# Kernel tuning notes

Hardware: AMD Instinct MI355X
Metric: run time of the kernel (lower is better)

The kernel has to match this reference:

```python
import jax, jax.numpy as jnp
import numpy as np

H, W = 352, 1216
K = 8                 # points_per_pixel (z-buffer depth)
RADIUS_PX = 1.5       # splat radius in pixels
RAD_POW = 2.0         # opts.rad_pow
TAU = 1.0             # opts.tau


def _rasterize(pts):
    # pts: [B,P,3] with xy in NDC [-1,1], z>0.
    # Returns idx [B,H,W,K] int32 (packed point index, -1 = empty),
    # dist2 [B,H,W,K] squared NDC distance to pixel center, and NDC radius r.
    B, P, _ = pts.shape
    r = RADIUS_PX / max(H, W) * 2.0
    hx = int(np.ceil(r * W / 2.0))   # splat half-extent in pixels (x)
    hy = int(np.ceil(r * H / 2.0))   # splat half-extent in pixels (y)
    dy, dx = np.meshgrid(np.arange(-hy, hy + 1), np.arange(-hx, hx + 1), indexing='ij')
    dy = jnp.asarray(dy.ravel()); dx = jnp.asarray(dx.ravel())     # [Wn]
    x, y, z = pts[..., 0], pts[..., 1], pts[..., 2]                # [B,P]
    i0 = jnp.floor((y + 1.0) * 0.5 * H).astype(jnp.int32)
    j0 = jnp.floor((x + 1.0) * 0.5 * W).astype(jnp.int32)
    ii = i0[..., None] + dy                                        # [B,P,Wn]
    jj = j0[..., None] + dx
    xc = (jj + 0.5) * (2.0 / W) - 1.0                              # pixel centers (NDC)
    yc = (ii + 0.5) * (2.0 / H) - 1.0
    d2 = (x[..., None] - xc) ** 2 + (y[..., None] - yc) ** 2
    valid = (ii >= 0) & (ii < H) & (jj >= 0) & (jj < W) & (d2 < r * r) & (z[..., None] > 0)
    NPIX = B * H * W
    pix = jnp.where(valid, (jnp.arange(B)[:, None, None] * H + ii) * W + jj, NPIX)
    pid = jnp.broadcast_to((jnp.arange(B)[:, None] * P + jnp.arange(P)[None, :])[..., None], pix.shape)
    pixf = pix.reshape(-1)
    zf = jnp.broadcast_to(z[..., None], pix.shape).reshape(-1)
    d2f = d2.reshape(-1)
    pidf = pid.reshape(-1)
    # sort candidates by (pixel, z): gives nearest-first z-buffer ordering per pixel
    order = jnp.lexsort((zf, pixf))
    pixs, d2s, pids = pixf[order], d2f[order], pidf[order]
    first = jnp.searchsorted(pixs, pixs, side='left')
    rank = jnp.arange(pixs.shape[0]) - first      # z-rank within each pixel
    keep = (rank < K) & (pixs < NPIX)
    tp = jnp.where(keep, pixs, NPIX)              # sentinel row NPIX collects rejects
    tr = jnp.where(keep, rank, 0)
    idx = jnp.full((NPIX + 1, K), -1, jnp.int32).at[tp, tr].set(
        jnp.where(keep, pids, -1).astype(jnp.int32))
    dist2 = jnp.zeros((NPIX + 1, K), pts.dtype).at[tp, tr].set(
        jnp.where(keep, d2s, jnp.zeros((), pts.dtype)))
    return idx[:NPIX].reshape(B, H, W, K), dist2[:NPIX].reshape(B, H, W, K), r


def _forward(pts3D, src):
    B, C, P = src.shape
    idx, dist2, r = _rasterize(pts3D)
    dist = dist2 / (r ** RAD_POW)
    alphas = (1.0 - jnp.sqrt(jnp.clip(dist, 0.001, 1.0))) ** TAU   # [B,H,W,K]
    feats = src.transpose(0, 2, 1).reshape(B * P, C)               # features_packed [B*P,C]
    acc = jnp.zeros((B, H, W, C), src.dtype)
    for k in range(K):   # fixed small depth-layer loop: weighted_sum compositing
        ik = idx[..., k]
        wk = jnp.where(ik >= 0, alphas[..., k], 0.0)
        acc = acc + wk[..., None] * feats[jnp.clip(ik, 0)]
    return acc.transpose(0, 3, 1, 2)                               # [B,C,H,W]


def setup_inputs():
    key = jax.random.key(0)
    k1, k2, k3 = jax.random.split(key, 3)
    B, P, C = 2, 65536, 64
    xy = jax.random.uniform(k1, (B, P, 2), minval=-1.0, maxval=1.0)
    z = jax.random.uniform(k2, (B, P, 1), minval=0.5, maxval=20.0)
    pts3D = jnp.concatenate([xy, z], axis=-1)
    src = jax.random.normal(k3, (B, C, P), dtype=jnp.float32)
    return {"pts3D": pts3D, "src": src}


def reference(pts3D, src):
    return _forward(pts3D, src)
```

## Files before the change

### kernel.cpp

```cpp
#include <hip/hip_runtime.h>
#include <cstdint>
#include <cstddef>

#define HH 352
#define WW 1216
#define KK 8
#define PP 65536
#define BB 2
#define CC 64

#define RD (1.5 / 1216.0 * 2.0)


__global__ __launch_bounds__(256) void scatter_kernel(const float* __restrict__ pts,
                                                      unsigned int* __restrict__ slots) {
    const int tid = blockIdx.x * blockDim.x + threadIdx.x;
    const int b = tid >> 16;
    const float x = pts[tid * 3 + 0];
    const float y = pts[tid * 3 + 1];
    const float z = pts[tid * 3 + 2];
    if (!(z > 0.f)) return;

    const int i0 = (int)floorf((y + 1.f) * 0.5f * (float)HH);
    if (i0 < 0 || i0 >= HH) return;
    const int j0 = (int)floorf((x + 1.f) * 0.5f * (float)WW);

    const float yc = ((float)i0 + 0.5f) * (2.f / (float)HH) - 1.f;
    const float dyv = y - yc;
    const float dy2 = dyv * dyv;
    const float r2 = (float)(RD * RD);

    unsigned int fb = __float_as_uint(z) >> 13;
    fb = fb < 0x1F800u ? 0x1F800u : fb;
    fb = fb > 0x217FFu ? 0x217FFu : fb;
    const unsigned int key = ((fb - 0x1F800u) << 17) | (unsigned int)tid;

    const unsigned int rowbase = (unsigned int)(b * HH + i0) * WW;

    #pragma unroll
    for (int dx = -1; dx <= 1; ++dx) {
        const int jj = j0 + dx;
        if (jj < 0 || jj >= WW) continue;
        const float xc = ((float)jj + 0.5f) * (2.f / (float)WW) - 1.f;
        const float dxv = x - xc;
        if (!(dxv * dxv + dy2 < r2)) continue;

        unsigned int* s = slots + (size_t)(rowbase + jj) * KK;
        unsigned int cur = key;
        #pragma unroll
        for (int k = 0; k < KK; ++k) {
            unsigned int old = atomicMin(&s[k], cur);
            if (old & 0x80000000u) break;
            cur = old > cur ? old : cur;
        }
    }
}

__global__ __launch_bounds__(256) void transpose_src(const float* __restrict__ src,
                                                     float* __restrict__ feats) {
    __shared__ float tile[64][65];
    const int b  = blockIdx.y;
    const int p0 = blockIdx.x * 64;
    const float* sb = src + (size_t)b * CC * PP;
    #pragma unroll
    for (int i = 0; i < 16; ++i) {
        const int idx = threadIdx.x + i * 256;
        const int c = idx >> 6;
        const int p = idx & 63;
        tile[p][c] = sb[(size_t)c * PP + (p0 + p)];
    }
    __syncthreads();
    float* fbp = feats + ((size_t)b * PP + p0) * CC;
    #pragma unroll
    for (int i = 0; i < 16; ++i) {
        const int idx = threadIdx.x + i * 256;
        const int p = idx >> 6;
        const int c = idx & 63;
        fbp[(size_t)p * CC + c] = tile[p][c];
    }
}

__global__ __launch_bounds__(256) void composite_kernel(const float* __restrict__ pts,
                                                        const float* __restrict__ feats,
                                                        const unsigned int* __restrict__ slots,
                                                        float* __restrict__ out) {
    const int HWp = HH * WW;
    const int tid = blockIdx.x * blockDim.x + threadIdx.x;
    const int b = tid / HWp;
    const int hw = tid - b * HWp;
    const int h = hw / WW;
    const int w = hw - h * WW;

    const uint4* sv = (const uint4*)(slots + (size_t)tid * KK);
    const uint4 sa = sv[0], sb4 = sv[1];
    const unsigned int keys[KK] = {sa.x, sa.y, sa.z, sa.w, sb4.x, sb4.y, sb4.z, sb4.w};

    float* ob = out + (size_t)b * CC * HWp + hw;

    if (keys[0] & 0x80000000u) {
        #pragma unroll
        for (int c = 0; c < CC; ++c)
            __builtin_nontemporal_store(0.f, ob + (size_t)c * HWp);
        return;
    }

    const float xc = ((float)w + 0.5f) * (2.f / (float)WW) - 1.f;
    const float yc = ((float)h + 0.5f) * (2.f / (float)HH) - 1.f;
    const float invr2 = (float)(1.0 / (RD * RD));

    float acc[CC];
    #pragma unroll
    for (int c = 0; c < CC; ++c) acc[c] = 0.f;

    #pragma unroll
    for (int k = 0; k < KK; ++k) {
        const unsigned int key = keys[k];
        if (key & 0x80000000u) break;
        const int pid = (int)(key & 0x1FFFFu);
        const float px = pts[pid * 3 + 0];
        const float py = pts[pid * 3 + 1];
        const float ddx = px - xc;
        const float ddy = py - yc;
        float dist = (ddx * ddx + ddy * ddy) * invr2;
        dist = fminf(fmaxf(dist, 0.001f), 1.0f);
        const float a = 1.f - sqrtf(dist);

        const float4* f = (const float4*)(feats + (size_t)pid * CC);
        #pragma unroll
        for (int j = 0; j < CC / 4; ++j) {
            const float4 v = f[j];
            acc[4 * j + 0] += a * v.x;
            acc[4 * j + 1] += a * v.y;
            acc[4 * j + 2] += a * v.z;
            acc[4 * j + 3] += a * v.w;
        }
    }

    #pragma unroll
    for (int c = 0; c < CC; ++c)
        __builtin_nontemporal_store(acc[c], ob + (size_t)c * HWp);
}

__global__ __launch_bounds__(256) void composite_direct(const float* __restrict__ pts,
                                                        const float* __restrict__ src,
                                                        const unsigned int* __restrict__ slots,
                                                        float* __restrict__ out) {
    const int HWp = HH * WW;
    const int tid = blockIdx.x * blockDim.x + threadIdx.x;
    const int b = tid / HWp;
    const int hw = tid - b * HWp;
    const int h = hw / WW;
    const int w = hw - h * WW;

    const uint4* sv = (const uint4*)(slots + (size_t)tid * KK);
    const uint4 sa = sv[0], sb4 = sv[1];
    const unsigned int keys[KK] = {sa.x, sa.y, sa.z, sa.w, sb4.x, sb4.y, sb4.z, sb4.w};

    const float xc = ((float)w + 0.5f) * (2.f / (float)WW) - 1.f;
    const float yc = ((float)h + 0.5f) * (2.f / (float)HH) - 1.f;
    const float invr2 = (float)(1.0 / (RD * RD));

    float alpha[KK];
    int   pidx[KK];
    int n = 0;
    #pragma unroll
    for (int k = 0; k < KK; ++k) {
        const unsigned int key = keys[k];
        if (key & 0x80000000u) break;
        const int pid = (int)(key & 0x1FFFFu);
        const float px = pts[pid * 3 + 0];
        const float py = pts[pid * 3 + 1];
        const float ddx = px - xc;
        const float ddy = py - yc;
        float dist = (ddx * ddx + ddy * ddy) * invr2;
        dist = fminf(fmaxf(dist, 0.001f), 1.0f);
        alpha[k] = 1.f - sqrtf(dist);
        pidx[k]  = pid & (PP - 1);
        n = k + 1;
    }

    const float* sbp = src + (size_t)b * CC * PP;
    float* ob = out + (size_t)b * CC * HWp + hw;
    for (int c = 0; c < CC; ++c) {
        float acc = 0.f;
        #pragma unroll
        for (int k = 0; k < KK; ++k)
            if (k < n) acc += alpha[k] * sbp[(size_t)c * PP + pidx[k]];
        __builtin_nontemporal_store(acc, ob + (size_t)c * HWp);
    }
}

extern "C" void kernel_launch(void* const* d_in, const int* in_sizes, int n_in,
                              void* d_out, int out_size, void* d_ws, size_t ws_size,
                              hipStream_t stream) {
    const float* pts = (const float*)d_in[0];
    const float* src = (const float*)d_in[1];
    float* out = (float*)d_out;

    const size_t slot_bytes  = (size_t)BB * HH * WW * KK * sizeof(unsigned int);
    const size_t feats_bytes = (size_t)BB * PP * CC * sizeof(float);
    const size_t need = slot_bytes + feats_bytes;

    const int npix_blocks = (BB * HH * WW) / 256;

    if (ws_size >= need + 256) {
        char* base = (char*)d_ws + ((ws_size - need) & ~(size_t)255);
        float* feats = (float*)base;
        unsigned int* slots = (unsigned int*)(base + feats_bytes);

        scatter_kernel<<<(BB * PP) / 256, 256, 0, stream>>>(pts, slots);
        transpose_src<<<dim3(PP / 64, BB), 256, 0, stream>>>(src, feats);
        composite_kernel<<<npix_blocks, 256, 0, stream>>>(pts, feats, slots, out);
    } else {
        unsigned int* slots = (unsigned int*)d_ws;
        scatter_kernel<<<(BB * PP) / 256, 256, 0, stream>>>(pts, slots);
        composite_direct<<<npix_blocks, 256, 0, stream>>>(pts, src, slots, out);
    }
}
```

Baseline: 269.6 us.

## Store transposed features as bf16 and fuse transpose with scatter

The transpose now packs features into bf16 pairs, halving the bytes the composite kernel gathers per point. The transpose and scatter kernels are merged into one launch with block-index dispatch, so both run concurrently and one launch is saved. The empty-pixel early-exit in compositing is removed, so empty pixels run the normal loop and store zeros. The cost is bf16 rounding of the features, which reduces output precision.

```diff
diff --git a/kernel.cpp b/kernel.cpp
--- a/kernel.cpp
+++ b/kernel.cpp
@@ -12,9 +12,16 @@
 #define RD (1.5 / 1216.0 * 2.0)
 
 
-__global__ __launch_bounds__(256) void scatter_kernel(const float* __restrict__ pts,
-                                                      unsigned int* __restrict__ slots) {
-    const int tid = blockIdx.x * blockDim.x + threadIdx.x;
+static __device__ __forceinline__ unsigned int bf16pack_rn(float a, float b) {
+    unsigned int ua = __float_as_uint(a), ub = __float_as_uint(b);
+    ua = (ua + 0x7FFFu + ((ua >> 16) & 1u)) >> 16;
+    ub = (ub + 0x7FFFu + ((ub >> 16) & 1u)) >> 16;
+    return (ub << 16) | ua;
+}
+
+static __device__ __forceinline__ void scatter_body(const float* __restrict__ pts,
+                                                    unsigned int* __restrict__ slots,
+                                                    int tid) {
     const int b = tid >> 16;
     const float x = pts[tid * 3 + 0];
     const float y = pts[tid * 3 + 1];
@@ -56,32 +63,47 @@
     }
 }
 
-__global__ __launch_bounds__(256) void transpose_src(const float* __restrict__ src,
-                                                     float* __restrict__ feats) {
+#define TRANS_BLOCKS (BB * (PP / 64))
+#define SCATTER_BLOCKS ((BB * PP) / 256)
+
+__global__ __launch_bounds__(256) void prep_kernel(const float* __restrict__ pts,
+                                                   const float* __restrict__ src,
+                                                   unsigned int* __restrict__ slots,
+                                                   unsigned int* __restrict__ feats) {
     __shared__ float tile[64][65];
-    const int b  = blockIdx.y;
-    const int p0 = blockIdx.x * 64;
-    const float* sb = src + (size_t)b * CC * PP;
-    #pragma unroll
-    for (int i = 0; i < 16; ++i) {
-        const int idx = threadIdx.x + i * 256;
-        const int c = idx >> 6;
-        const int p = idx & 63;
-        tile[p][c] = sb[(size_t)c * PP + (p0 + p)];
-    }
-    __syncthreads();
-    float* fbp = feats + ((size_t)b * PP + p0) * CC;
-    #pragma unroll
-    for (int i = 0; i < 16; ++i) {
-        const int idx = threadIdx.x + i * 256;
-        const int p = idx >> 6;
-        const int c = idx & 63;
-        fbp[(size_t)p * CC + c] = tile[p][c];
-    }
+    if (blockIdx.x < TRANS_BLOCKS) {
+        const int bid = blockIdx.x;
+        const int b = bid >> 10;
+        const int p0 = (bid & 1023) * 64;
+        const float* sb = src + (size_t)b * CC * PP;
+        #pragma unroll
+        for (int i = 0; i < 16; ++i) {
+            const int idx = threadIdx.x + i * 256;
+            const int c = idx >> 6;
+            const int p = idx & 63;
+            tile[p][c] = sb[(size_t)c * PP + (p0 + p)];
+        }
+        __syncthreads();
+        unsigned int* fbp = feats + ((size_t)b * PP + p0) * (CC / 2);
+        #pragma unroll
+        for (int i = 0; i < 8; ++i) {
+            const int idx = threadIdx.x + i * 256;
+            const int p = idx >> 5;
+            const int cp = idx & 31;
+            fbp[(size_t)p * (CC / 2) + cp] = bf16pack_rn(tile[p][2 * cp], tile[p][2 * cp + 1]);
+        }
+        return;
+    }
+    scatter_body(pts, slots, (blockIdx.x - TRANS_BLOCKS) * 256 + threadIdx.x);
+}
+
+__global__ __launch_bounds__(256) void scatter_kernel(const float* __restrict__ pts,
+                                                      unsigned int* __restrict__ slots) {
+    scatter_body(pts, slots, blockIdx.x * 256 + threadIdx.x);
 }
 
 __global__ __launch_bounds__(256) void composite_kernel(const float* __restrict__ pts,
-                                                        const float* __restrict__ feats,
+                                                        const unsigned int* __restrict__ feats,
                                                         const unsigned int* __restrict__ slots,
                                                         float* __restrict__ out) {
     const int HWp = HH * WW;
@@ -94,15 +116,6 @@
     const uint4* sv = (const uint4*)(slots + (size_t)tid * KK);
     const uint4 sa = sv[0], sb4 = sv[1];
     const unsigned int keys[KK] = {sa.x, sa.y, sa.z, sa.w, sb4.x, sb4.y, sb4.z, sb4.w};
-
-    float* ob = out + (size_t)b * CC * HWp + hw;
-
-    if (keys[0] & 0x80000000u) {
-        #pragma unroll
-        for (int c = 0; c < CC; ++c)
-            __builtin_nontemporal_store(0.f, ob + (size_t)c * HWp);
-        return;
-    }
 
     const float xc = ((float)w + 0.5f) * (2.f / (float)WW) - 1.f;
     const float yc = ((float)h + 0.5f) * (2.f / (float)HH) - 1.f;
@@ -125,17 +138,22 @@
         dist = fminf(fmaxf(dist, 0.001f), 1.0f);
         const float a = 1.f - sqrtf(dist);
 
-        const float4* f = (const float4*)(feats + (size_t)pid * CC);
-        #pragma unroll
-        for (int j = 0; j < CC / 4; ++j) {
-            const float4 v = f[j];
-            acc[4 * j + 0] += a * v.x;
-            acc[4 * j + 1] += a * v.y;
-            acc[4 * j + 2] += a * v.z;
-            acc[4 * j + 3] += a * v.w;
-        }
-    }
-
+        const uint4* f = (const uint4*)(feats + (size_t)pid * (CC / 2));
+        #pragma unroll
+        for (int j = 0; j < CC / 8; ++j) {
+            const uint4 q = f[j];
+            acc[8 * j + 0] += a * __uint_as_float(q.x << 16);
+            acc[8 * j + 1] += a * __uint_as_float(q.x & 0xFFFF0000u);
+            acc[8 * j + 2] += a * __uint_as_float(q.y << 16);
+            acc[8 * j + 3] += a * __uint_as_float(q.y & 0xFFFF0000u);
+            acc[8 * j + 4] += a * __uint_as_float(q.z << 16);
+            acc[8 * j + 5] += a * __uint_as_float(q.z & 0xFFFF0000u);
+            acc[8 * j + 6] += a * __uint_as_float(q.w << 16);
+            acc[8 * j + 7] += a * __uint_as_float(q.w & 0xFFFF0000u);
+        }
+    }
+
+    float* ob = out + (size_t)b * CC * HWp + hw;
     #pragma unroll
     for (int c = 0; c < CC; ++c)
         __builtin_nontemporal_store(acc[c], ob + (size_t)c * HWp);
@@ -198,22 +216,21 @@
     float* out = (float*)d_out;
 
     const size_t slot_bytes  = (size_t)BB * HH * WW * KK * sizeof(unsigned int);
-    const size_t feats_bytes = (size_t)BB * PP * CC * sizeof(float);
+    const size_t feats_bytes = (size_t)BB * PP * CC * 2;
     const size_t need = slot_bytes + feats_bytes;
 
     const int npix_blocks = (BB * HH * WW) / 256;
 
     if (ws_size >= need + 256) {
         char* base = (char*)d_ws + ((ws_size - need) & ~(size_t)255);
-        float* feats = (float*)base;
+        unsigned int* feats = (unsigned int*)base;
         unsigned int* slots = (unsigned int*)(base + feats_bytes);
 
-        scatter_kernel<<<(BB * PP) / 256, 256, 0, stream>>>(pts, slots);
-        transpose_src<<<dim3(PP / 64, BB), 256, 0, stream>>>(src, feats);
+        prep_kernel<<<TRANS_BLOCKS + SCATTER_BLOCKS, 256, 0, stream>>>(pts, src, slots, feats);
         composite_kernel<<<npix_blocks, 256, 0, stream>>>(pts, feats, slots, out);
     } else {
         unsigned int* slots = (unsigned int*)d_ws;
-        scatter_kernel<<<(BB * PP) / 256, 256, 0, stream>>>(pts, slots);
+        scatter_kernel<<<SCATTER_BLOCKS, 256, 0, stream>>>(pts, slots);
         composite_direct<<<npix_blocks, 256, 0, stream>>>(pts, src, slots, out);
     }
 }
```

Measured after the change: 260.2 us. 1.04x faster.
